# Optimization experiments

Hardware: AMD Instinct MI355X
Metric: run time of the kernel (lower is better)

Reference implementation:

```python
import jax, jax.numpy as jnp
import numpy as np

B, H, W, C = 64, 14, 14, 768
HID = 4 * C            # ConvNeXt MLP hidden
E, K, R = 8, 2, 16     # num_experts, top_k, lora rank
SCALING = 16.0 / 16.0  # alpha / r


def setup_inputs() -> dict:
    key = jax.random.key(0)
    ks = jax.random.split(key, 9)
    N = B * H * W
    x = jax.random.normal(ks[0], (B, H, W, C), jnp.float32)
    p = jax.random.uniform(ks[1], (N, K), jnp.float32)
    topk_probs = p / (p.sum(-1, keepdims=True) + 1e-6)
    topk_idx = jax.random.randint(ks[2], (N, K), 0, E)
    w1 = jax.random.normal(ks[3], (C, HID), jnp.float32) * (C ** -0.5)
    b1 = jnp.zeros((HID,), jnp.float32)
    w2 = jax.random.normal(ks[4], (HID, C), jnp.float32) * (HID ** -0.5)
    b2 = jnp.zeros((C,), jnp.float32)
    w_down = jax.random.normal(ks[5], (E, C, R), jnp.float32) * (C ** -0.5)
    # torch init is zeros; use small randn so the op is numerically non-trivial
    w_up = jax.random.normal(ks[6], (E, R, C), jnp.float32) * 0.02
    return {"x": x, "topk_probs": topk_probs, "topk_idx": topk_idx,
            "w1": w1, "b1": b1, "w2": w2, "b2": b2,
            "w_down": w_down, "w_up": w_up}


def reference(x, topk_probs, topk_idx, w1, b1, w2, b2, w_down, w_up):
    # orig ConvNeXt MLP: Linear -> GELU(exact) -> Linear, pointwise over [B,H,W,C]
    h = jax.nn.gelu(jnp.einsum('bhwc,cf->bhwf', x, w1) + b1, approximate=False)
    orig = jnp.einsum('bhwf,fc->bhwc', h, w2) + b2

    N = x.shape[0] * x.shape[1] * x.shape[2]
    xf = x.reshape(N, C)  # [N, C] tokens
    # per-token combine weight for each expert: sum_k p[n,k] * 1[idx[n,k]==e]
    wt = (jax.nn.one_hot(topk_idx, E, dtype=xf.dtype) * topk_probs[..., None]).sum(1)  # [N, E]
    # dense-over-experts LoRA (vectorized form of the per-expert gather/scatter loop)
    down = jax.nn.gelu(jnp.einsum('nc,ecr->ner', xf, w_down), approximate=False)  # [N, E, R]
    up = jnp.einsum('ner,erc->nec', down, w_up) * SCALING                          # [N, E, C]
    moe = jnp.einsum('nec,ne->nc', up, wt)                                         # [N, C]
    return orig + moe.reshape(x.shape)
```

## Files before the change

kernel.cpp:

```cpp
#include <hip/hip_runtime.h>
#include <hip/hip_bf16.h>
#include <math.h>


#define NTOK   12544
#define CDIM   768
#define HIDDIM 3072
#define KBIG   3200

typedef __attribute__((ext_vector_type(8))) short bf16x8;
typedef __attribute__((ext_vector_type(4))) float f32x4;

#define GLOBAL_AS(p) ((const __attribute__((address_space(1))) void*)(p))
#define LDS_AS(p)    ((__attribute__((address_space(3))) void*)(p))

__device__ inline unsigned short f2bf(float f) {
    unsigned int x = __float_as_uint(f);
    x += 0x7fffu + ((x >> 16) & 1u);
    return (unsigned short)(x >> 16);
}

__device__ inline float gelu_fast(float x) {
    float x3 = x * x * x;
    float u2 = 1.5957691216057308f * x + 0.07135481627260025f * x3;
    float e = __expf(-u2);
    return x * __builtin_amdgcn_rcpf(1.0f + e);
}

__global__ void __launch_bounds__(256) prep_kernel(
        const float* __restrict__ x, const float* __restrict__ w1,
        const float* __restrict__ w2, const float* __restrict__ wup,
        const float* __restrict__ wdn,
        unsigned short* __restrict__ xb, unsigned short* __restrict__ w1t,
        unsigned short* __restrict__ B2t, unsigned short* __restrict__ wdt) {
    __shared__ float tile[64][65];
    const int b = blockIdx.x, tid = threadIdx.x;
    if (b < 9408) {
        int i = b * 256 + tid;
        float4 v = ((const float4*)x)[i];
        ushort4 o;
        o.x = f2bf(v.x); o.y = f2bf(v.y); o.z = f2bf(v.z); o.w = f2bf(v.w);
        ((ushort4*)xb)[i] = o;
        return;
    }
    if (b < 10584) {
        const float* in; unsigned short* outp; int Ccols, out_ld, out_off, bx, by;
        if (b < 9984)       { int t = b - 9408;  in = w1;  outp = w1t; Ccols = 3072; out_ld = 768;  out_off = 0;    bx = t % 48; by = t / 48; }
        else if (b < 10560) { int t = b - 9984;  in = w2;  outp = B2t; Ccols = 768;  out_ld = 3200; out_off = 0;    bx = t % 12; by = t / 12; }
        else                { int t = b - 10560; in = wup; outp = B2t; Ccols = 768;  out_ld = 3200; out_off = 3072; bx = t % 12; by = t / 12; }
        const int c0 = bx * 64, r0 = by * 64;
        #pragma unroll
        for (int p = 0; p < 4; ++p) {
            int idx = p * 256 + tid;
            int r = idx >> 4, c4 = (idx & 15) * 4;
            float4 v = *(const float4*)&in[(size_t)(r0 + r) * Ccols + c0 + c4];
            tile[r][c4 + 0] = v.x; tile[r][c4 + 1] = v.y;
            tile[r][c4 + 2] = v.z; tile[r][c4 + 3] = v.w;
        }
        __syncthreads();
        #pragma unroll
        for (int p = 0; p < 2; ++p) {
            int u = p * 256 + tid;
            int cc = u >> 3, r8 = (u & 7) * 8;
            uint4 pk;
            pk.x = (unsigned)f2bf(tile[r8 + 0][cc]) | ((unsigned)f2bf(tile[r8 + 1][cc]) << 16);
            pk.y = (unsigned)f2bf(tile[r8 + 2][cc]) | ((unsigned)f2bf(tile[r8 + 3][cc]) << 16);
            pk.z = (unsigned)f2bf(tile[r8 + 4][cc]) | ((unsigned)f2bf(tile[r8 + 5][cc]) << 16);
            pk.w = (unsigned)f2bf(tile[r8 + 6][cc]) | ((unsigned)f2bf(tile[r8 + 7][cc]) << 16);
            *(uint4*)&outp[(size_t)(c0 + cc) * out_ld + out_off + r0 + r8] = pk;
        }
        return;
    }
    {
        int idx = (b - 10584) * 256 + tid;
        int j = idx / 768, c = idx - j * 768;
        int e = j >> 4, r = j & 15;
        wdt[idx] = f2bf(wdn[((size_t)e * 768 + c) * 16 + r]);
    }
}


template <int EPI, int TM>
__global__ void __launch_bounds__(TM * 2)
gemm_bt_kernel(const unsigned short* __restrict__ A, int lda,
               const unsigned short* __restrict__ Bt, int ldb,
               int kIters,
               const float* __restrict__ bias,
               unsigned short* __restrict__ apOut,
               float* __restrict__ fOut,
               const int* __restrict__ tki,
               const float* __restrict__ tkp) {
    constexpr int NT    = TM * 2;
    constexpr int ABUF  = TM * 32;
    constexpr int BBUF  = 128 * 32;
    __shared__ __align__(16) unsigned short As[2 * ABUF];
    __shared__ __align__(16) unsigned short Bs[2 * BBUF];

    int bx, by;
    if (EPI == 2) {
        int L = blockIdx.x;
        int k = L & 7, t = L >> 3;
        bx = t % 6;
        by = (t / 6) * 8 + k;
        if (by >= NTOK / 128) return;
    } else {
        bx = blockIdx.x;
        by = blockIdx.y;
    }

    const int tid  = threadIdx.x;
    const int wave = tid >> 6;
    const int lane = tid & 63;
    const int m0 = by * TM;
    const int n0 = bx * 128;
    const int wm = (wave >> 1) * 64;
    const int wn = (wave & 1) * 64;
    const int row16 = lane & 15;
    const int quad  = lane >> 4;
    const int kch   = quad * 8;

    f32x4 acc[4][4] = {};

    const int r_s = tid >> 2;
    const int c_s = (tid & 3) * 8;
    const size_t aRow0 = (size_t)(m0 + r_s) * lda + c_s;
    const size_t aRow1 = aRow0 + (size_t)(NT / 4) * lda;
    const size_t bRow0 = (size_t)(n0 + r_s) * ldb + c_s;
    const size_t bRow1 = bRow0 + (size_t)64 * ldb;
    unsigned short* asB0 = &As[(wave * 64) * 8];
    unsigned short* asB1 = &As[(NT + wave * 64) * 8];
    unsigned short* bsB0 = &Bs[(wave * 64) * 8];
    unsigned short* bsB1 = &Bs[(256 + wave * 64) * 8];

    {
        __builtin_amdgcn_global_load_lds(GLOBAL_AS(A + aRow0), LDS_AS(asB0), 16, 0, 0);
        __builtin_amdgcn_global_load_lds(GLOBAL_AS(A + aRow1), LDS_AS(asB1), 16, 0, 0);
        __builtin_amdgcn_global_load_lds(GLOBAL_AS(Bt + bRow0), LDS_AS(bsB0), 16, 0, 0);
        if (TM == 128)
            __builtin_amdgcn_global_load_lds(GLOBAL_AS(Bt + bRow1), LDS_AS(bsB1), 16, 0, 0);
    }

    for (int kt = 0; kt < kIters; ++kt) {
        __syncthreads();

        if (kt + 1 < kIters) {
            const int k1 = (kt + 1) * 32;
            const int pa = ((kt + 1) & 1) * ABUF;
            const int pb = ((kt + 1) & 1) * BBUF;
            __builtin_amdgcn_global_load_lds(GLOBAL_AS(A + aRow0 + k1), LDS_AS(asB0 + pa), 16, 0, 0);
            __builtin_amdgcn_global_load_lds(GLOBAL_AS(A + aRow1 + k1), LDS_AS(asB1 + pa), 16, 0, 0);
            __builtin_amdgcn_global_load_lds(GLOBAL_AS(Bt + bRow0 + k1), LDS_AS(bsB0 + pb), 16, 0, 0);
            if (TM == 128)
                __builtin_amdgcn_global_load_lds(GLOBAL_AS(Bt + bRow1 + k1), LDS_AS(bsB1 + pb), 16, 0, 0);
        }

        const int ca = (kt & 1) * ABUF;
        const int cb = (kt & 1) * BBUF;
        bf16x8 af[4], bfr[4];
        #pragma unroll
        for (int mi = 0; mi < 4; ++mi)
            af[mi] = *(const bf16x8*)&As[ca + (wm + mi * 16 + row16) * 32 + kch];
        #pragma unroll
        for (int ni = 0; ni < 4; ++ni)
            bfr[ni] = *(const bf16x8*)&Bs[cb + (wn + ni * 16 + row16) * 32 + kch];

        #pragma unroll
        for (int mi = 0; mi < 4; ++mi)
            #pragma unroll
            for (int ni = 0; ni < 4; ++ni)
                acc[mi][ni] = __builtin_amdgcn_mfma_f32_16x16x32_bf16(
                    af[mi], bfr[ni], acc[mi][ni], 0, 0, 0);
    }

    #pragma unroll
    for (int mi = 0; mi < 4; ++mi) {
        #pragma unroll
        for (int i = 0; i < 4; ++i) {
            const int m = m0 + wm + mi * 16 + quad * 4 + i;
            int i0 = 0, i1 = 0; float p0 = 0.f, p1 = 0.f;
            if (EPI == 1) {
                i0 = tki[m * 2]; i1 = tki[m * 2 + 1];
                p0 = tkp[m * 2]; p1 = tkp[m * 2 + 1];
            }
            #pragma unroll
            for (int ni = 0; ni < 4; ++ni) {
                const int ncol = n0 + wn + ni * 16 + row16;
                float v = acc[mi][ni][i];
                if (EPI == 0) {
                    v = gelu_fast(v + bias[ncol]);
                    apOut[(size_t)m * KBIG + ncol] = f2bf(v);
                } else if (EPI == 1) {
                    const int e = ncol >> 4;
                    float wt = (i0 == e ? p0 : 0.f) + (i1 == e ? p1 : 0.f);
                    v = gelu_fast(v) * wt;
                    apOut[(size_t)m * KBIG + 3072 + ncol] = f2bf(v);
                } else {
                    fOut[(size_t)m * CDIM + ncol] = v + bias[ncol];
                }
            }
        }
    }
}


extern "C" void kernel_launch(void* const* d_in, const int* in_sizes, int n_in,
                              void* d_out, int out_size, void* d_ws, size_t ws_size,
                              hipStream_t stream) {
    const float* x   = (const float*)d_in[0];
    const float* tkp = (const float*)d_in[1];
    const int*   tki = (const int*)d_in[2];
    const float* w1  = (const float*)d_in[3];
    const float* b1  = (const float*)d_in[4];
    const float* w2  = (const float*)d_in[5];
    const float* b2  = (const float*)d_in[6];
    const float* wdn = (const float*)d_in[7];
    const float* wup = (const float*)d_in[8];
    float* out = (float*)d_out;

    unsigned short* xb  = (unsigned short*)d_ws;
    unsigned short* w1t = xb  + (size_t)NTOK * CDIM;
    unsigned short* B2t = w1t + (size_t)HIDDIM * CDIM;
    unsigned short* wdt = B2t + (size_t)CDIM * KBIG;
    unsigned short* Ap  = wdt + (size_t)128 * CDIM;

    prep_kernel<<<dim3(10968), 256, 0, stream>>>(x, w1, w2, wup, wdn,
                                                 xb, w1t, B2t, wdt);

    gemm_bt_kernel<1, 128><<<dim3(1, NTOK / 128), 256, 0, stream>>>(
        xb, CDIM, wdt, CDIM, CDIM / 32, nullptr, Ap, nullptr, tki, tkp);
    gemm_bt_kernel<0, 256><<<dim3(HIDDIM / 128, NTOK / 256), 512, 0, stream>>>(
        xb, CDIM, w1t, CDIM, CDIM / 32, b1, Ap, nullptr, nullptr, nullptr);
    gemm_bt_kernel<2, 128><<<dim3(624), 256, 0, stream>>>(
        Ap, KBIG, B2t, KBIG, KBIG / 32, b2, nullptr, out, nullptr, nullptr);
}
```

Baseline: 303.6 us.

## Fuse LoRA-down GEMM into first MLP GEMM launch and shrink second GEMM tiles

The separate LoRA down-projection launch is folded into the first GEMM as an extra 25th column block. That block reads the LoRA weights and applies the gated GELU epilogue. The second GEMM moves from 128-row tiles with 256 threads to 64-row tiles with 128 threads, launching more blocks for better occupancy and tail balance. Load loops are generalized by tile size. Smaller tiles in the big K=3200 GEMM lower operand reuse and add more B traffic.

New measurement: 327.4 us. 7.9% more time.

```diff
diff --git a/kernel.cpp b/kernel.cpp
--- a/kernel.cpp
+++ b/kernel.cpp
@@ -89,10 +89,12 @@
                unsigned short* __restrict__ apOut,
                float* __restrict__ fOut,
                const int* __restrict__ tki,
-               const float* __restrict__ tkp) {
+               const float* __restrict__ tkp,
+               const unsigned short* __restrict__ Bt2) {
     constexpr int NT    = TM * 2;
     constexpr int ABUF  = TM * 32;
     constexpr int BBUF  = 128 * 32;
+    constexpr int BPASS = BBUF / (NT * 8);
     __shared__ __align__(16) unsigned short As[2 * ABUF];
     __shared__ __align__(16) unsigned short Bs[2 * BBUF];
 
@@ -102,17 +104,20 @@
         int k = L & 7, t = L >> 3;
         bx = t % 6;
         by = (t / 6) * 8 + k;
-        if (by >= NTOK / 128) return;
+        if (by >= NTOK / TM) return;
     } else {
         bx = blockIdx.x;
         by = blockIdx.y;
     }
+
+    const unsigned short* Bp = Bt;
+    int n0 = bx * 128;
+    if (EPI == 3 && bx == 24) { Bp = Bt2; n0 = 0; }
 
     const int tid  = threadIdx.x;
     const int wave = tid >> 6;
     const int lane = tid & 63;
     const int m0 = by * TM;
-    const int n0 = bx * 128;
     const int wm = (wave >> 1) * 64;
     const int wn = (wave & 1) * 64;
     const int row16 = lane & 15;
@@ -124,21 +129,18 @@
     const int r_s = tid >> 2;
     const int c_s = (tid & 3) * 8;
     const size_t aRow0 = (size_t)(m0 + r_s) * lda + c_s;
-    const size_t aRow1 = aRow0 + (size_t)(NT / 4) * lda;
     const size_t bRow0 = (size_t)(n0 + r_s) * ldb + c_s;
-    const size_t bRow1 = bRow0 + (size_t)64 * ldb;
-    unsigned short* asB0 = &As[(wave * 64) * 8];
-    unsigned short* asB1 = &As[(NT + wave * 64) * 8];
-    unsigned short* bsB0 = &Bs[(wave * 64) * 8];
-    unsigned short* bsB1 = &Bs[(256 + wave * 64) * 8];
-
-    {
-        __builtin_amdgcn_global_load_lds(GLOBAL_AS(A + aRow0), LDS_AS(asB0), 16, 0, 0);
-        __builtin_amdgcn_global_load_lds(GLOBAL_AS(A + aRow1), LDS_AS(asB1), 16, 0, 0);
-        __builtin_amdgcn_global_load_lds(GLOBAL_AS(Bt + bRow0), LDS_AS(bsB0), 16, 0, 0);
-        if (TM == 128)
-            __builtin_amdgcn_global_load_lds(GLOBAL_AS(Bt + bRow1), LDS_AS(bsB1), 16, 0, 0);
-    }
+    unsigned short* asBase = &As[wave * 512];
+    unsigned short* bsBase = &Bs[wave * 512];
+
+    #pragma unroll
+    for (int p = 0; p < 2; ++p)
+        __builtin_amdgcn_global_load_lds(GLOBAL_AS(A + aRow0 + (size_t)p * (NT / 4) * lda),
+                                         LDS_AS(asBase + p * NT * 8), 16, 0, 0);
+    #pragma unroll
+    for (int p = 0; p < BPASS; ++p)
+        __builtin_amdgcn_global_load_lds(GLOBAL_AS(Bp + bRow0 + (size_t)p * (NT / 4) * ldb),
+                                         LDS_AS(bsBase + p * NT * 8), 16, 0, 0);
 
     for (int kt = 0; kt < kIters; ++kt) {
         __syncthreads();
@@ -147,11 +149,14 @@
             const int k1 = (kt + 1) * 32;
             const int pa = ((kt + 1) & 1) * ABUF;
             const int pb = ((kt + 1) & 1) * BBUF;
-            __builtin_amdgcn_global_load_lds(GLOBAL_AS(A + aRow0 + k1), LDS_AS(asB0 + pa), 16, 0, 0);
-            __builtin_amdgcn_global_load_lds(GLOBAL_AS(A + aRow1 + k1), LDS_AS(asB1 + pa), 16, 0, 0);
-            __builtin_amdgcn_global_load_lds(GLOBAL_AS(Bt + bRow0 + k1), LDS_AS(bsB0 + pb), 16, 0, 0);
-            if (TM == 128)
-                __builtin_amdgcn_global_load_lds(GLOBAL_AS(Bt + bRow1 + k1), LDS_AS(bsB1 + pb), 16, 0, 0);
+            #pragma unroll
+            for (int p = 0; p < 2; ++p)
+                __builtin_amdgcn_global_load_lds(GLOBAL_AS(A + aRow0 + k1 + (size_t)p * (NT / 4) * lda),
+                                                 LDS_AS(asBase + pa + p * NT * 8), 16, 0, 0);
+            #pragma unroll
+            for (int p = 0; p < BPASS; ++p)
+                __builtin_amdgcn_global_load_lds(GLOBAL_AS(Bp + bRow0 + k1 + (size_t)p * (NT / 4) * ldb),
+                                                 LDS_AS(bsBase + pb + p * NT * 8), 16, 0, 0);
         }
 
         const int ca = (kt & 1) * ABUF;
@@ -172,13 +177,14 @@
                     af[mi], bfr[ni], acc[mi][ni], 0, 0, 0);
     }
 
+    const bool doLora = (EPI == 1) || (EPI == 3 && bx == 24);
     #pragma unroll
     for (int mi = 0; mi < 4; ++mi) {
         #pragma unroll
         for (int i = 0; i < 4; ++i) {
             const int m = m0 + wm + mi * 16 + quad * 4 + i;
             int i0 = 0, i1 = 0; float p0 = 0.f, p1 = 0.f;
-            if (EPI == 1) {
+            if (doLora) {
                 i0 = tki[m * 2]; i1 = tki[m * 2 + 1];
                 p0 = tkp[m * 2]; p1 = tkp[m * 2 + 1];
             }
@@ -186,16 +192,16 @@
             for (int ni = 0; ni < 4; ++ni) {
                 const int ncol = n0 + wn + ni * 16 + row16;
                 float v = acc[mi][ni][i];
-                if (EPI == 0) {
-                    v = gelu_fast(v + bias[ncol]);
-                    apOut[(size_t)m * KBIG + ncol] = f2bf(v);
-                } else if (EPI == 1) {
+                if (EPI == 2) {
+                    fOut[(size_t)m * CDIM + ncol] = v + bias[ncol];
+                } else if (doLora) {
                     const int e = ncol >> 4;
                     float wt = (i0 == e ? p0 : 0.f) + (i1 == e ? p1 : 0.f);
                     v = gelu_fast(v) * wt;
                     apOut[(size_t)m * KBIG + 3072 + ncol] = f2bf(v);
                 } else {
-                    fOut[(size_t)m * CDIM + ncol] = v + bias[ncol];
+                    v = gelu_fast(v + bias[ncol]);
+                    apOut[(size_t)m * KBIG + ncol] = f2bf(v);
                 }
             }
         }
@@ -226,10 +232,8 @@
     prep_kernel<<<dim3(10968), 256, 0, stream>>>(x, w1, w2, wup, wdn,
                                                  xb, w1t, B2t, wdt);
 
-    gemm_bt_kernel<1, 128><<<dim3(1, NTOK / 128), 256, 0, stream>>>(
-        xb, CDIM, wdt, CDIM, CDIM / 32, nullptr, Ap, nullptr, tki, tkp);
-    gemm_bt_kernel<0, 256><<<dim3(HIDDIM / 128, NTOK / 256), 512, 0, stream>>>(
-        xb, CDIM, w1t, CDIM, CDIM / 32, b1, Ap, nullptr, nullptr, nullptr);
-    gemm_bt_kernel<2, 128><<<dim3(624), 256, 0, stream>>>(
-        Ap, KBIG, B2t, KBIG, KBIG / 32, b2, nullptr, out, nullptr, nullptr);
-}
+    gemm_bt_kernel<3, 256><<<dim3(25, NTOK / 256), 512, 0, stream>>>(
+        xb, CDIM, w1t, CDIM, CDIM / 32, b1, Ap, nullptr, tki, tkp, wdt);
+    gemm_bt_kernel<2, 64><<<dim3(1200), 128, 0, stream>>>(
+        Ap, KBIG, B2t, KBIG, KBIG / 32, b2, nullptr, out, nullptr, nullptr, nullptr);
+}
```

## Replace big GEMMs with 256x256 eight-wave phased pipelined kernel

Applied to the files above, without the earlier changes.

Adds a new GEMM kernel that uses 256x256 output tiles, 8 waves, 64-wide K tiles, swizzled LDS layout and an 8-phase schedule. Each phase interleaves async global-to-LDS loads with MFMA bursts, using explicit barriers, waitcnt and setprio. It replaces both the hidden-layer GEMM and the output GEMM. The goal is more reuse per tile and better overlap of memory and compute. The trade-offs are higher register and LDS pressure, removal of the grouped block ordering for the second GEMM, and a fragile hand-written synchronisation scheme.

Result: no change. 307.2 us (+1.2%).

```diff
diff --git a/kernel.cpp b/kernel.cpp
--- a/kernel.cpp
+++ b/kernel.cpp
@@ -13,6 +13,7 @@
 
 #define GLOBAL_AS(p) ((const __attribute__((address_space(1))) void*)(p))
 #define LDS_AS(p)    ((__attribute__((address_space(3))) void*)(p))
+#define GLD(src, dst) __builtin_amdgcn_global_load_lds(GLOBAL_AS(src), LDS_AS(dst), 16, 0, 0)
 
 __device__ inline unsigned short f2bf(float f) {
     unsigned int x = __float_as_uint(f);
@@ -79,7 +80,6 @@
     }
 }
 
-
 template <int EPI, int TM>
 __global__ void __launch_bounds__(TM * 2)
 gemm_bt_kernel(const unsigned short* __restrict__ A, int lda,
@@ -96,18 +96,7 @@
     __shared__ __align__(16) unsigned short As[2 * ABUF];
     __shared__ __align__(16) unsigned short Bs[2 * BBUF];
 
-    int bx, by;
-    if (EPI == 2) {
-        int L = blockIdx.x;
-        int k = L & 7, t = L >> 3;
-        bx = t % 6;
-        by = (t / 6) * 8 + k;
-        if (by >= NTOK / 128) return;
-    } else {
-        bx = blockIdx.x;
-        by = blockIdx.y;
-    }
-
+    const int bx = blockIdx.x, by = blockIdx.y;
     const int tid  = threadIdx.x;
     const int wave = tid >> 6;
     const int lane = tid & 63;
@@ -133,11 +122,10 @@
     unsigned short* bsB1 = &Bs[(256 + wave * 64) * 8];
 
     {
-        __builtin_amdgcn_global_load_lds(GLOBAL_AS(A + aRow0), LDS_AS(asB0), 16, 0, 0);
-        __builtin_amdgcn_global_load_lds(GLOBAL_AS(A + aRow1), LDS_AS(asB1), 16, 0, 0);
-        __builtin_amdgcn_global_load_lds(GLOBAL_AS(Bt + bRow0), LDS_AS(bsB0), 16, 0, 0);
-        if (TM == 128)
-            __builtin_amdgcn_global_load_lds(GLOBAL_AS(Bt + bRow1), LDS_AS(bsB1), 16, 0, 0);
+        GLD(A + aRow0, asB0);
+        GLD(A + aRow1, asB1);
+        GLD(Bt + bRow0, bsB0);
+        if (TM == 128) GLD(Bt + bRow1, bsB1);
     }
 
     for (int kt = 0; kt < kIters; ++kt) {
@@ -147,11 +135,10 @@
             const int k1 = (kt + 1) * 32;
             const int pa = ((kt + 1) & 1) * ABUF;
             const int pb = ((kt + 1) & 1) * BBUF;
-            __builtin_amdgcn_global_load_lds(GLOBAL_AS(A + aRow0 + k1), LDS_AS(asB0 + pa), 16, 0, 0);
-            __builtin_amdgcn_global_load_lds(GLOBAL_AS(A + aRow1 + k1), LDS_AS(asB1 + pa), 16, 0, 0);
-            __builtin_amdgcn_global_load_lds(GLOBAL_AS(Bt + bRow0 + k1), LDS_AS(bsB0 + pb), 16, 0, 0);
-            if (TM == 128)
-                __builtin_amdgcn_global_load_lds(GLOBAL_AS(Bt + bRow1 + k1), LDS_AS(bsB1 + pb), 16, 0, 0);
+            GLD(A + aRow0 + k1, asB0 + pa);
+            GLD(A + aRow1 + k1, asB1 + pa);
+            GLD(Bt + bRow0 + k1, bsB0 + pb);
+            if (TM == 128) GLD(Bt + bRow1 + k1, bsB1 + pb);
         }
 
         const int ca = (kt & 1) * ABUF;
@@ -203,6 +190,136 @@
 }
 
 
+template <int Q, bool TAILV, class Issue>
+__device__ __forceinline__ void phase8(
+        const char* ldsAbuf, const char* ldsBbuf, int aFB, int bFB,
+        f32x4 (&acc)[8][4], bf16x8 (&bfr)[4][2], Issue issue) {
+    bf16x8 af[2][2];
+    #pragma unroll
+    for (int f = 0; f < 2; ++f)
+        #pragma unroll
+        for (int k = 0; k < 2; ++k)
+            af[f][k] = *(const bf16x8*)(ldsAbuf + aFB + Q * 4096 + f * 2048 + k * 64);
+    if (Q == 0) {
+        #pragma unroll
+        for (int nf = 0; nf < 4; ++nf)
+            #pragma unroll
+            for (int k = 0; k < 2; ++k)
+                bfr[nf][k] = *(const bf16x8*)(ldsBbuf + bFB + nf * 2048 + k * 64);
+    }
+    issue();
+    __builtin_amdgcn_s_barrier();
+    asm volatile("s_waitcnt lgkmcnt(0)" ::: "memory");
+    __builtin_amdgcn_sched_barrier(0);
+    __builtin_amdgcn_s_setprio(1);
+    #pragma unroll
+    for (int f = 0; f < 2; ++f)
+        #pragma unroll
+        for (int nf = 0; nf < 4; ++nf)
+            #pragma unroll
+            for (int k = 0; k < 2; ++k)
+                acc[2 * Q + f][nf] = __builtin_amdgcn_mfma_f32_16x16x32_bf16(
+                    af[f][k], bfr[nf][k], acc[2 * Q + f][nf], 0, 0, 0);
+    __builtin_amdgcn_s_setprio(0);
+    if (TAILV) asm volatile("s_waitcnt vmcnt(4)" ::: "memory");
+    __builtin_amdgcn_s_barrier();
+    __builtin_amdgcn_sched_barrier(0);
+}
+
+template <int EPI>
+__global__ void __launch_bounds__(512, 2)
+gemm8_kernel(const unsigned short* __restrict__ A, int lda,
+             const unsigned short* __restrict__ Bt, int ldb,
+             int kTiles, const float* __restrict__ bias,
+             unsigned short* __restrict__ apOut, float* __restrict__ fOut) {
+    __shared__ __align__(1024) unsigned short ldsbuf[65536];
+    char* ldsA = (char*)ldsbuf;
+    char* ldsB = (char*)ldsbuf + 65536;
+
+    const int tid  = threadIdx.x;
+    const int wave = tid >> 6;
+    const int lane = tid & 63;
+    const int m0 = blockIdx.y * 256;
+    const int n0 = blockIdx.x * 256;
+    const int row16 = lane & 15;
+    const int quad  = lane >> 4;
+    const int wm = (wave >> 2) << 7;
+    const int wn = (wave & 3) << 6;
+    const int swz = ((row16 >> 2) & 1) << 5;
+    const int aFB = (((wm + row16) << 7) + (quad << 4)) ^ swz;
+    const int bFB = (((wn + row16) << 7) + (quad << 4)) ^ swz;
+
+    const int d  = tid << 4;
+    const int s  = d ^ (((d >> 9) & 1) << 5);
+    const int sr = s >> 7;
+    const int sc = (s & 127) >> 1;
+    const char* aSrc = (const char*)(A + (size_t)(m0 + sr) * lda + sc);
+    const char* bSrc = (const char*)(Bt + (size_t)(n0 + sr) * ldb + sc);
+    const size_t aPass = (size_t)64 * lda * 2, aHalf = aPass * 2;
+    const size_t bPass = (size_t)64 * ldb * 2, bHalf = bPass * 2;
+    const int ldsW = wave << 10;
+
+    auto issueA = [&](int b, int h, int tk) {
+        const char* sp = aSrc + (size_t)h * aHalf + (size_t)tk * 128;
+        char* dp = ldsA + b * 32768 + h * 16384 + ldsW;
+        GLD(sp, dp);
+        GLD(sp + aPass, dp + 8192);
+    };
+    auto issueB = [&](int b, int h, int tk) {
+        const char* sp = bSrc + (size_t)h * bHalf + (size_t)tk * 128;
+        char* dp = ldsB + b * 32768 + h * 16384 + ldsW;
+        GLD(sp, dp);
+        GLD(sp + bPass, dp + 8192);
+    };
+
+    f32x4 acc[8][4] = {};
+
+    issueB(0, 0, 0); issueB(0, 1, 0);
+    issueA(0, 0, 0); issueA(0, 1, 0);
+    issueB(1, 0, 1); issueB(1, 1, 1);
+    asm volatile("s_waitcnt vmcnt(4)" ::: "memory");
+    __builtin_amdgcn_s_barrier();
+    __builtin_amdgcn_sched_barrier(0);
+
+    const char* A0 = ldsA;         const char* B0 = ldsB;
+    const char* A1 = ldsA + 32768; const char* B1 = ldsB + 32768;
+    const int nIter = kTiles >> 1;
+    for (int it = 0; it < nIter; ++it) {
+        const int t  = it * 2;
+        const int t2 = (t + 2 < kTiles) ? t + 2 : 0;
+        const int t3 = (t + 3 < kTiles) ? t + 3 : 0;
+        bf16x8 bfr[4][2];
+        phase8<0, false>(A0, B0, aFB, bFB, acc, bfr, [&]{ issueA(1, 0, t + 1); });
+        phase8<1, false>(A0, B0, aFB, bFB, acc, bfr, [&]{ issueA(1, 1, t + 1); });
+        phase8<2, false>(A0, B0, aFB, bFB, acc, bfr, [&]{ issueB(0, 0, t2); });
+        phase8<3, true >(A0, B0, aFB, bFB, acc, bfr, [&]{ issueB(0, 1, t2); });
+        phase8<0, false>(A1, B1, aFB, bFB, acc, bfr, [&]{ issueA(0, 0, t2); });
+        phase8<1, false>(A1, B1, aFB, bFB, acc, bfr, [&]{ issueA(0, 1, t2); });
+        phase8<2, false>(A1, B1, aFB, bFB, acc, bfr, [&]{ issueB(1, 0, t3); });
+        phase8<3, true >(A1, B1, aFB, bFB, acc, bfr, [&]{ issueB(1, 1, t3); });
+    }
+    asm volatile("s_waitcnt vmcnt(0)" ::: "memory");
+
+    float bv[4];
+    #pragma unroll
+    for (int nf = 0; nf < 4; ++nf) bv[nf] = bias[n0 + wn + nf * 16 + row16];
+    #pragma unroll
+    for (int mi = 0; mi < 8; ++mi) {
+        #pragma unroll
+        for (int i = 0; i < 4; ++i) {
+            const int m = m0 + wm + mi * 16 + quad * 4 + i;
+            #pragma unroll
+            for (int nf = 0; nf < 4; ++nf) {
+                const int col = n0 + wn + nf * 16 + row16;
+                float v = acc[mi][nf][i] + bv[nf];
+                if (EPI == 0) apOut[(size_t)m * KBIG + col] = f2bf(gelu_fast(v));
+                else          fOut[(size_t)m * CDIM + col] = v;
+            }
+        }
+    }
+}
+
+
 extern "C" void kernel_launch(void* const* d_in, const int* in_sizes, int n_in,
                               void* d_out, int out_size, void* d_ws, size_t ws_size,
                               hipStream_t stream) {
@@ -228,8 +345,8 @@
 
     gemm_bt_kernel<1, 128><<<dim3(1, NTOK / 128), 256, 0, stream>>>(
         xb, CDIM, wdt, CDIM, CDIM / 32, nullptr, Ap, nullptr, tki, tkp);
-    gemm_bt_kernel<0, 256><<<dim3(HIDDIM / 128, NTOK / 256), 512, 0, stream>>>(
-        xb, CDIM, w1t, CDIM, CDIM / 32, b1, Ap, nullptr, nullptr, nullptr);
-    gemm_bt_kernel<2, 128><<<dim3(624), 256, 0, stream>>>(
-        Ap, KBIG, B2t, KBIG, KBIG / 32, b2, nullptr, out, nullptr, nullptr);
-}
+    gemm8_kernel<0><<<dim3(HIDDIM / 256, NTOK / 256), 512, 0, stream>>>(
+        xb, CDIM, w1t, CDIM, CDIM / 64, b1, Ap, nullptr);
+    gemm8_kernel<2><<<dim3(CDIM / 256, NTOK / 256), 512, 0, stream>>>(
+        Ap, KBIG, B2t, KBIG, KBIG / 64, b2, nullptr, out);
+}
```
